# Optimization experiments

Hardware: AMD Instinct MI355X
Metric: run time of the kernel (lower is better)

Reference implementation:

```python
import jax, jax.numpy as jnp
import numpy as np
import math

LMAX = 2            # input lmax
LMAX_OUT = 2 * LMAX # gaunt product output lmax
RES_BETA = 20
RES_ALPHA = 39
N = 2048
MUL = 64
C = 64
BRANCHES = [(1, 1), (1, -1), (-1, 1)]  # (p_val1, p_val2) per branch


def _real_sh_grid(lmax, res_beta, res_alpha):
    """Real orthonormal spherical harmonics on a Gauss-Legendre x uniform-alpha grid.
    Returns Y [(lmax+1)^2, res_beta, res_alpha] and quadrature weights qw [res_beta]
    (beta GL weight times 2*pi/res_alpha alpha weight)."""
    x, w = np.polynomial.legendre.leggauss(res_beta)  # x = cos(beta)
    phi = np.linspace(0.0, 2.0 * np.pi, res_alpha, endpoint=False)
    # associated Legendre P[l, m] on x via standard recurrences
    P = np.zeros((lmax + 1, lmax + 1, res_beta))
    P[0, 0] = 1.0
    s = np.sqrt(1.0 - x ** 2)
    for m in range(1, lmax + 1):
        P[m, m] = -(2 * m - 1) * s * P[m - 1, m - 1]
    for m in range(lmax):
        P[m + 1, m] = (2 * m + 1) * x * P[m, m]
    for m in range(lmax + 1):
        for l in range(m + 2, lmax + 1):
            P[l, m] = ((2 * l - 1) * x * P[l - 1, m] - (l + m - 1) * P[l - 2, m]) / (l - m)
    Y = np.zeros(((lmax + 1) ** 2, res_beta, res_alpha))
    idx = 0
    for l in range(lmax + 1):
        for m in range(-l, l + 1):
            am = abs(m)
            K = math.sqrt((2 * l + 1) / (4 * math.pi) * math.factorial(l - am) / math.factorial(l + am))
            if m == 0:
                ang = np.ones(res_alpha)
            elif m > 0:
                ang = math.sqrt(2.0) * np.cos(m * phi)
            else:
                ang = math.sqrt(2.0) * np.sin(am * phi)
            Y[idx] = K * P[l, am][:, None] * ang[None, :]
            idx += 1
    qw = w * (2.0 * np.pi / res_alpha)
    return Y.astype(np.float32), qw.astype(np.float32)


def setup_inputs() -> dict:
    key = jax.random.key(0)
    k1, k2, k3, k4, k5 = jax.random.split(key, 5)
    # inputs carry both parities per l: [N, mul, parity(2), (lmax+1)^2]
    x1 = jax.random.normal(k1, (N, MUL, 2, (LMAX + 1) ** 2), dtype=jnp.float32)
    x2 = jax.random.normal(k2, (N, MUL, 2, (LMAX + 1) ** 2), dtype=jnp.float32)
    # per-branch, per-l linear weights (e3nn Linear mixes multiplicities within each irrep)
    W1 = jax.random.normal(k3, (3, LMAX + 1, MUL, C), dtype=jnp.float32)
    W2 = jax.random.normal(k4, (3, LMAX + 1, MUL, C), dtype=jnp.float32)
    Wout = jax.random.normal(k5, (3, LMAX_OUT + 1, C, C), dtype=jnp.float32)
    Yfull, qw = _real_sh_grid(LMAX_OUT, RES_BETA, RES_ALPHA)
    Y_in = jnp.asarray(Yfull[: (LMAX + 1) ** 2])   # [9, B, A]
    Y_out = jnp.asarray(Yfull)                     # [25, B, A]
    return {"x1": x1, "x2": x2, "W1": W1, "W2": W2, "Wout": Wout,
            "Y_in": Y_in, "Y_out": Y_out, "qw": jnp.asarray(qw)}


def _project(x, W, p_val):
    """e3nn Linear to s2_irreps(LMAX, p_val)*C: for each l, take the input block with
    parity p_val*(-1)^l and mix multiplicities. x [N,mul,2,L2], W [L, mul, C] -> [N, C, L2]."""
    blocks = []
    inv_sqrt_mul = 1.0 / np.sqrt(x.shape[1])
    for l in range(LMAX + 1):
        pidx = 0 if p_val * ((-1) ** l) == 1 else 1  # 0 = even, 1 = odd parity slot
        sl = slice(l * l, (l + 1) * (l + 1))
        blocks.append(jnp.einsum('nmk,mc->nck', x[:, :, pidx, sl], W[l]) * inv_sqrt_mul)
    return jnp.concatenate(blocks, axis=-1)  # [N, C, (LMAX+1)^2]


def _gaunt_branch(x1, x2, W1b, W2b, Woutb, p1, p2, Y_in, Y_out, qw):
    c1 = _project(x1, W1b, p1)                      # [N, C, 9]
    c2 = _project(x2, W2b, p2)
    # SH -> grid (inverse spherical transform)
    s1 = jnp.einsum('ncl,lba->ncba', c1, Y_in)      # [N, C, B, A]
    s2 = jnp.einsum('ncl,lba->ncba', c2, Y_in)
    # pointwise multiply on S2, then grid -> SH (forward transform w/ quadrature)
    co = jnp.einsum('ncba,lba,b->ncl', s1 * s2, Y_out, qw)  # [N, C, 25]
    # linear_out: per-l [C -> C] mixing
    inv_sqrt_c = 1.0 / np.sqrt(co.shape[1])
    outs = []
    for l in range(LMAX_OUT + 1):
        sl = slice(l * l, (l + 1) * (l + 1))
        outs.append(jnp.einsum('nck,cd->ndk', co[:, :, sl], Woutb[l]) * inv_sqrt_c)
    return jnp.concatenate(outs, axis=-1)           # [N, C, 25]


def reference(x1, x2, W1, W2, Wout, Y_in, Y_out, qw):
    outs = [_gaunt_branch(x1, x2, W1[b], W2[b], Wout[b], p1, p2, Y_in, Y_out, qw)
            for b, (p1, p2) in enumerate(BRANCHES)]
    return jnp.stack(outs, axis=1)                  # [N, 3, C, 25] (concat over parities)
```

## Files before the change

kernel.cpp:

```cpp
#include <hip/hip_runtime.h>
#include <utility>


#define NN 2048

__host__ __device__ constexpr int l_of9(int i)  { return i < 1 ? 0 : (i < 4 ? 1 : 2); }
__host__ __device__ constexpr int l_of25(int k) { return k < 1 ? 0 : (k < 4 ? 1 : (k < 9 ? 2 : (k < 16 ? 3 : 4))); }
__host__ __device__ constexpr int iabs_(int v)  { return v < 0 ? -v : v; }

__host__ __device__ constexpr bool gmask(int k, int i, int j) {
    const int l3 = l_of25(k), m3 = k - l3 * l3 - l3;
    const int l1 = l_of9(i),  m1 = i - l1 * l1 - l1;
    const int l2 = l_of9(j),  m2 = j - l2 * l2 - l2;
    if (((l1 + l2 + l3) & 1) != 0) return false;
    if (l3 > l1 + l2 || l3 < iabs_(l1 - l2)) return false;
    const int am3 = iabs_(m3);
    return (am3 == iabs_(m1 + m2)) || (am3 == iabs_(m1 - m2));
}

struct GTab {
    int po[82];
    int pc[81];
    int kl[81][12];
    constexpr GTab() : po{}, pc{}, kl{} {
        int off = 0;
        for (int ij = 0; ij < 81; ++ij) {
            po[ij] = off;
            const int i = ij / 9, j = ij % 9;
            int cnum = 0;
            for (int k = 0; k < 25; ++k)
                if (gmask(k, i, j)) kl[ij][cnum++] = k;
            pc[ij] = cnum;
            off += (cnum + 3) & ~3;
        }
        po[81] = off;
    }
};
constexpr GTab GT{};

__global__ __launch_bounds__(256) void gaunt_pack_kernel(
    const float* __restrict__ Y_in, const float* __restrict__ Y_out,
    const float* __restrict__ qw, float* __restrict__ gp)
{
    const int ij = blockIdx.x;
    const int i = ij / 9, j = ij % 9;
    const int t = threadIdx.x;

    __shared__ float yy[780];
    __shared__ float ps[25][8];
    __shared__ float gr[25];

    for (int p = t; p < 780; p += 256)
        yy[p] = Y_in[i * 780 + p] * Y_in[j * 780 + p] * qw[p / 39];
    __syncthreads();

    if (t < 200) {
        const int k = t >> 3, s = t & 7;
        const float* yo = Y_out + k * 780;
        const int p1 = (s * 98 + 98 < 780) ? (s * 98 + 98) : 780;
        float a = 0.f;
        for (int p = s * 98; p < p1; ++p) a = fmaf(yy[p], yo[p], a);
        ps[k][s] = a;
    }
    __syncthreads();

    if (t < 25) {
        float a = 0.f;
#pragma unroll
        for (int s = 0; s < 8; ++s) a += ps[t][s];
        gr[t] = a;
    }
    __syncthreads();

    const int cntp = (GT.pc[ij] + 3) & ~3;
    if (t < cntp)
        gp[GT.po[ij] + t] = (t < GT.pc[ij]) ? gr[GT.kl[ij][t]] : 0.f;
}

template <int IJ, int... Ts>
__device__ __forceinline__ void gaunt_apply(const float (&g)[12], float pij,
    float (&cov)[25], std::integer_sequence<int, Ts...>)
{
    ((cov[GT.kl[IJ][Ts]] = fmaf(g[Ts], pij, cov[GT.kl[IJ][Ts]])), ...);
}

template <int IJ>
__device__ __forceinline__ void gaunt_pair(const float* __restrict__ gp,
    const float (&c1)[9], const float (&c2)[9], float (&cov)[25])
{
    constexpr int cnt = GT.pc[IJ];
    if constexpr (cnt > 0) {
        constexpr int base = GT.po[IJ];
        constexpr int nv = (cnt + 3) / 4;
        const float pij = c1[IJ / 9] * c2[IJ % 9];
        float g[12];
#pragma unroll
        for (int q = 0; q < nv; ++q) {
            const float4 v = ((const float4*)(gp + base))[q];
            g[4 * q] = v.x; g[4 * q + 1] = v.y; g[4 * q + 2] = v.z; g[4 * q + 3] = v.w;
        }
        gaunt_apply<IJ>(g, pij, cov, std::make_integer_sequence<int, cnt>{});
    }
}

template <int I, int... Js>
__device__ __forceinline__ void gaunt_row(const float* __restrict__ gp,
    const float (&c1)[9], const float (&c2)[9], float (&cov)[25],
    std::integer_sequence<int, Js...>)
{
    (gaunt_pair<I * 9 + Js>(gp, c1, c2, cov), ...);
    __builtin_amdgcn_sched_barrier(0);
}

template <int... Is>
__device__ __forceinline__ void gaunt_all(const float* __restrict__ gp,
    const float (&c1)[9], const float (&c2)[9], float (&cov)[25],
    std::integer_sequence<int, Is...>)
{
    (gaunt_row<Is>(gp, c1, c2, cov, std::make_integer_sequence<int, 9>{}), ...);
}

template <int E1, int E2>
__device__ __forceinline__ void fused_body(
    const float* __restrict__ x1, const float* __restrict__ x2,
    const float* __restrict__ W1, const float* __restrict__ W2,
    const float* __restrict__ Wout, const float* __restrict__ gp,
    float* __restrict__ out, char* smem, int b)
{
    const int t = threadIdx.x;
    const int c = t & 63;
    const int w = t >> 6;
    const int n = blockIdx.x * 4 + w;

    float2* ws = (float2*)smem;
    float*  cs2 = (float*)smem;
    float*  cs  = (float*)(smem + 25600);

    const float* x1n = x1 + (size_t)n * 1152;
    const float* x2n = x2 + (size_t)n * 1152;

    float a1[9] = {0,0,0,0,0,0,0,0,0};
    float a2[9] = {0,0,0,0,0,0,0,0,0};

    for (int mc = 0; mc < 4; ++mc) {
        if (mc) __syncthreads();
        for (int idx = t; idx < 3072; idx += 256) {
            const int l = idx >> 10;
            const int r = idx & 1023;
            const int gi = ((b * 3 + l) * 64 + (mc * 16 + (r >> 6))) * 64 + (r & 63);
            ws[idx] = make_float2(W1[gi], W2[gi]);
        }
        __syncthreads();

#pragma unroll 1
        for (int mp = 0; mp < 8; ++mp) {
            const int m0 = mc * 16 + mp * 2;
            const float4* p1 = (const float4*)(x1n + m0 * 18);
            const float4* p2 = (const float4*)(x2n + m0 * 18);
            float xs1[36], xs2[36];
#pragma unroll
            for (int q = 0; q < 9; ++q) {
                const float4 t1 = p1[q], t2 = p2[q];
                xs1[4*q] = t1.x; xs1[4*q+1] = t1.y; xs1[4*q+2] = t1.z; xs1[4*q+3] = t1.w;
                xs2[4*q] = t2.x; xs2[4*q+1] = t2.y; xs2[4*q+2] = t2.z; xs2[4*q+3] = t2.w;
            }
            float2 wv[3][2];
#pragma unroll
            for (int l = 0; l < 3; ++l)
#pragma unroll
                for (int mi = 0; mi < 2; ++mi)
                    wv[l][mi] = ws[(l * 16 + mp * 2 + mi) * 64 + c];
#pragma unroll
            for (int l = 0; l < 3; ++l) {
                const int O1 = ((l & 1) ^ E1) * 9 + l * l;
                const int O2 = ((l & 1) ^ E2) * 9 + l * l;
#pragma unroll
                for (int mi = 0; mi < 2; ++mi)
#pragma unroll
                    for (int ii = 0; ii <= 2 * l; ++ii) {
                        a1[l*l+ii] = fmaf(xs1[O1 + 18*mi + ii], wv[l][mi].x, a1[l*l+ii]);
                        a2[l*l+ii] = fmaf(xs2[O2 + 18*mi + ii], wv[l][mi].y, a2[l*l+ii]);
                    }
            }
        }
    }
    __syncthreads();

    float c1[9], c2[9];
#pragma unroll
    for (int i = 0; i < 9; ++i) { c1[i] = a1[i] * 0.125f; c2[i] = a2[i] * 0.125f; }

    float cov[25] = {0,0,0,0,0,0,0,0,0,0,0,0,0,0,0,0,0,0,0,0,0,0,0,0,0};
    gaunt_all(gp, c1, c2, cov, std::make_integer_sequence<int, 9>{});

    float* csw = cs + w * (64 * 20);
    const float* WoB = Wout + (size_t)b * 5 * 4096 + c;

#pragma unroll
    for (int kk = 0; kk < 13; ++kk) csw[c * 20 + kk] = cov[kk];
    float accA[13];
#pragma unroll
    for (int kk = 0; kk < 13; ++kk) accA[kk] = 0.f;
#pragma unroll 2
    for (int d = 0; d < 64; ++d) {
        const float4 cv0 = *(const float4*)&csw[d * 20 + 0];
        const float4 cv1 = *(const float4*)&csw[d * 20 + 4];
        const float4 cv2 = *(const float4*)&csw[d * 20 + 8];
        const float4 cv3 = *(const float4*)&csw[d * 20 + 12];
        const float wv0 = WoB[(0 * 64 + d) * 64];
        const float wv1 = WoB[(1 * 64 + d) * 64];
        const float wv2 = WoB[(2 * 64 + d) * 64];
        const float wv3 = WoB[(3 * 64 + d) * 64];
        accA[0]  = fmaf(cv0.x, wv0, accA[0]);
        accA[1]  = fmaf(cv0.y, wv1, accA[1]);
        accA[2]  = fmaf(cv0.z, wv1, accA[2]);
        accA[3]  = fmaf(cv0.w, wv1, accA[3]);
        accA[4]  = fmaf(cv1.x, wv2, accA[4]);
        accA[5]  = fmaf(cv1.y, wv2, accA[5]);
        accA[6]  = fmaf(cv1.z, wv2, accA[6]);
        accA[7]  = fmaf(cv1.w, wv2, accA[7]);
        accA[8]  = fmaf(cv2.x, wv2, accA[8]);
        accA[9]  = fmaf(cv2.y, wv3, accA[9]);
        accA[10] = fmaf(cv2.z, wv3, accA[10]);
        accA[11] = fmaf(cv2.w, wv3, accA[11]);
        accA[12] = fmaf(cv3.x, wv3, accA[12]);
    }
#pragma unroll
    for (int kk = 0; kk < 13; ++kk)
        cs2[w * 1600 + c * 25 + kk] = accA[kk] * 0.125f;

#pragma unroll
    for (int kk = 0; kk < 12; ++kk) csw[c * 20 + kk] = cov[13 + kk];
    float accB[12];
#pragma unroll
    for (int kk = 0; kk < 12; ++kk) accB[kk] = 0.f;
#pragma unroll 2
    for (int d = 0; d < 64; ++d) {
        const float4 cv0 = *(const float4*)&csw[d * 20 + 0];
        const float4 cv1 = *(const float4*)&csw[d * 20 + 4];
        const float4 cv2 = *(const float4*)&csw[d * 20 + 8];
        const float wv3 = WoB[(3 * 64 + d) * 64];
        const float wv4 = WoB[(4 * 64 + d) * 64];
        accB[0]  = fmaf(cv0.x, wv3, accB[0]);
        accB[1]  = fmaf(cv0.y, wv3, accB[1]);
        accB[2]  = fmaf(cv0.z, wv3, accB[2]);
        accB[3]  = fmaf(cv0.w, wv4, accB[3]);
        accB[4]  = fmaf(cv1.x, wv4, accB[4]);
        accB[5]  = fmaf(cv1.y, wv4, accB[5]);
        accB[6]  = fmaf(cv1.z, wv4, accB[6]);
        accB[7]  = fmaf(cv1.w, wv4, accB[7]);
        accB[8]  = fmaf(cv2.x, wv4, accB[8]);
        accB[9]  = fmaf(cv2.y, wv4, accB[9]);
        accB[10] = fmaf(cv2.z, wv4, accB[10]);
        accB[11] = fmaf(cv2.w, wv4, accB[11]);
    }
#pragma unroll
    for (int kk = 0; kk < 12; ++kk)
        cs2[w * 1600 + c * 25 + 13 + kk] = accB[kk] * 0.125f;

    float* outn = out + ((size_t)n * 3 + b) * 1600;
#pragma unroll
    for (int r = 0; r < 6; ++r) {
        const float4 v = *(const float4*)&cs2[w * 1600 + r * 256 + c * 4];
        *(float4*)&outn[r * 256 + c * 4] = v;
    }
    outn[1536 + c] = cs2[w * 1600 + 1536 + c];
}

__global__ __launch_bounds__(256) void fused_kernel(
    const float* __restrict__ x1, const float* __restrict__ x2,
    const float* __restrict__ W1, const float* __restrict__ W2,
    const float* __restrict__ Wout, const float* __restrict__ gp,
    float* __restrict__ out)
{
    __shared__ __align__(16) char smem[46080];
    const int b = blockIdx.y;
    if (b == 0)      fused_body<0, 0>(x1, x2, W1, W2, Wout, gp, out, smem, 0);
    else if (b == 1) fused_body<0, 1>(x1, x2, W1, W2, Wout, gp, out, smem, 1);
    else             fused_body<1, 0>(x1, x2, W1, W2, Wout, gp, out, smem, 2);
}

extern "C" void kernel_launch(void* const* d_in, const int* in_sizes, int n_in,
                              void* d_out, int out_size, void* d_ws, size_t ws_size,
                              hipStream_t stream) {
    const float* x1    = (const float*)d_in[0];
    const float* x2    = (const float*)d_in[1];
    const float* W1    = (const float*)d_in[2];
    const float* W2    = (const float*)d_in[3];
    const float* Wout  = (const float*)d_in[4];
    const float* Y_in  = (const float*)d_in[5];
    const float* Y_out = (const float*)d_in[6];
    const float* qw    = (const float*)d_in[7];
    float* outp = (float*)d_out;
    float* gp   = (float*)d_ws;

    gaunt_pack_kernel<<<81, 256, 0, stream>>>(Y_in, Y_out, qw, gp);
    fused_kernel<<<dim3(NN / 4, 3), 256, 0, stream>>>(x1, x2, W1, W2, Wout, gp, outp);
}
```

Baseline: 157.8 us.

## Drop shared-memory weight staging, read W1/W2 directly, single-pass output projection

Removes the cooperative LDS staging of W1/W2 and its block-wide barriers, so each thread reads its weight column straight from global memory (cached in L2). The output linear stage becomes one 25-wide accumulation pass over a padded per-wave shared buffer instead of two passes, and results are written directly to global without an LDS transpose. Shared memory shrinks from 45 KB to 28 KB and launch bounds request 5 blocks per CU to raise occupancy. The trade-off is more register pressure from 25 accumulators and uncoalesced per-thread 25-float output stores.

```diff
diff --git a/kernel.cpp b/kernel.cpp
--- a/kernel.cpp
+++ b/kernel.cpp
@@ -125,66 +125,54 @@
     const float* __restrict__ x1, const float* __restrict__ x2,
     const float* __restrict__ W1, const float* __restrict__ W2,
     const float* __restrict__ Wout, const float* __restrict__ gp,
-    float* __restrict__ out, char* smem, int b)
+    float* __restrict__ out, float* __restrict__ cs, int b)
 {
     const int t = threadIdx.x;
     const int c = t & 63;
-    const int w = t >> 6;
+    const int w = __builtin_amdgcn_readfirstlane(t >> 6);
     const int n = blockIdx.x * 4 + w;
-
-    float2* ws = (float2*)smem;
-    float*  cs2 = (float*)smem;
-    float*  cs  = (float*)(smem + 25600);
 
     const float* x1n = x1 + (size_t)n * 1152;
     const float* x2n = x2 + (size_t)n * 1152;
+    const float* W1b = W1 + (size_t)b * 3 * 4096 + c;
+    const float* W2b = W2 + (size_t)b * 3 * 4096 + c;
 
     float a1[9] = {0,0,0,0,0,0,0,0,0};
     float a2[9] = {0,0,0,0,0,0,0,0,0};
 
-    for (int mc = 0; mc < 4; ++mc) {
-        if (mc) __syncthreads();
-        for (int idx = t; idx < 3072; idx += 256) {
-            const int l = idx >> 10;
-            const int r = idx & 1023;
-            const int gi = ((b * 3 + l) * 64 + (mc * 16 + (r >> 6))) * 64 + (r & 63);
-            ws[idx] = make_float2(W1[gi], W2[gi]);
-        }
-        __syncthreads();
-
 #pragma unroll 1
-        for (int mp = 0; mp < 8; ++mp) {
-            const int m0 = mc * 16 + mp * 2;
-            const float4* p1 = (const float4*)(x1n + m0 * 18);
-            const float4* p2 = (const float4*)(x2n + m0 * 18);
-            float xs1[36], xs2[36];
-#pragma unroll
-            for (int q = 0; q < 9; ++q) {
-                const float4 t1 = p1[q], t2 = p2[q];
-                xs1[4*q] = t1.x; xs1[4*q+1] = t1.y; xs1[4*q+2] = t1.z; xs1[4*q+3] = t1.w;
-                xs2[4*q] = t2.x; xs2[4*q+1] = t2.y; xs2[4*q+2] = t2.z; xs2[4*q+3] = t2.w;
+    for (int mp = 0; mp < 32; ++mp) {
+        const float4* p1 = (const float4*)(x1n + mp * 36);
+        const float4* p2 = (const float4*)(x2n + mp * 36);
+        float xs1[36], xs2[36];
+#pragma unroll
+        for (int q = 0; q < 9; ++q) {
+            const float4 t1 = p1[q], t2 = p2[q];
+            xs1[4*q] = t1.x; xs1[4*q+1] = t1.y; xs1[4*q+2] = t1.z; xs1[4*q+3] = t1.w;
+            xs2[4*q] = t2.x; xs2[4*q+1] = t2.y; xs2[4*q+2] = t2.z; xs2[4*q+3] = t2.w;
+        }
+        float w1v[3][2], w2v[3][2];
+#pragma unroll
+        for (int l = 0; l < 3; ++l)
+#pragma unroll
+            for (int mi = 0; mi < 2; ++mi) {
+                const int moff = (l * 64 + mp * 2 + mi) * 64;
+                w1v[l][mi] = W1b[moff];
+                w2v[l][mi] = W2b[moff];
             }
-            float2 wv[3][2];
-#pragma unroll
-            for (int l = 0; l < 3; ++l)
-#pragma unroll
-                for (int mi = 0; mi < 2; ++mi)
-                    wv[l][mi] = ws[(l * 16 + mp * 2 + mi) * 64 + c];
-#pragma unroll
-            for (int l = 0; l < 3; ++l) {
-                const int O1 = ((l & 1) ^ E1) * 9 + l * l;
-                const int O2 = ((l & 1) ^ E2) * 9 + l * l;
-#pragma unroll
-                for (int mi = 0; mi < 2; ++mi)
-#pragma unroll
-                    for (int ii = 0; ii <= 2 * l; ++ii) {
-                        a1[l*l+ii] = fmaf(xs1[O1 + 18*mi + ii], wv[l][mi].x, a1[l*l+ii]);
-                        a2[l*l+ii] = fmaf(xs2[O2 + 18*mi + ii], wv[l][mi].y, a2[l*l+ii]);
-                    }
-            }
-        }
-    }
-    __syncthreads();
+#pragma unroll
+        for (int l = 0; l < 3; ++l) {
+            const int O1 = ((l & 1) ^ E1) * 9 + l * l;
+            const int O2 = ((l & 1) ^ E2) * 9 + l * l;
+#pragma unroll
+            for (int mi = 0; mi < 2; ++mi)
+#pragma unroll
+                for (int ii = 0; ii <= 2 * l; ++ii) {
+                    a1[l*l+ii] = fmaf(xs1[O1 + 18*mi + ii], w1v[l][mi], a1[l*l+ii]);
+                    a2[l*l+ii] = fmaf(xs2[O2 + 18*mi + ii], w2v[l][mi], a2[l*l+ii]);
+                }
+        }
+    }
 
     float c1[9], c2[9];
 #pragma unroll
@@ -193,91 +181,47 @@
     float cov[25] = {0,0,0,0,0,0,0,0,0,0,0,0,0,0,0,0,0,0,0,0,0,0,0,0,0};
     gaunt_all(gp, c1, c2, cov, std::make_integer_sequence<int, 9>{});
 
-    float* csw = cs + w * (64 * 20);
+    float* csw = cs + w * (64 * 28);
+#pragma unroll
+    for (int kk = 0; kk < 25; ++kk) csw[c * 28 + kk] = cov[kk];
+
     const float* WoB = Wout + (size_t)b * 5 * 4096 + c;
-
-#pragma unroll
-    for (int kk = 0; kk < 13; ++kk) csw[c * 20 + kk] = cov[kk];
-    float accA[13];
-#pragma unroll
-    for (int kk = 0; kk < 13; ++kk) accA[kk] = 0.f;
-#pragma unroll 2
+    float acc[25];
+#pragma unroll
+    for (int kk = 0; kk < 25; ++kk) acc[kk] = 0.f;
+
+#pragma unroll 1
     for (int d = 0; d < 64; ++d) {
-        const float4 cv0 = *(const float4*)&csw[d * 20 + 0];
-        const float4 cv1 = *(const float4*)&csw[d * 20 + 4];
-        const float4 cv2 = *(const float4*)&csw[d * 20 + 8];
-        const float4 cv3 = *(const float4*)&csw[d * 20 + 12];
-        const float wv0 = WoB[(0 * 64 + d) * 64];
-        const float wv1 = WoB[(1 * 64 + d) * 64];
-        const float wv2 = WoB[(2 * 64 + d) * 64];
-        const float wv3 = WoB[(3 * 64 + d) * 64];
-        accA[0]  = fmaf(cv0.x, wv0, accA[0]);
-        accA[1]  = fmaf(cv0.y, wv1, accA[1]);
-        accA[2]  = fmaf(cv0.z, wv1, accA[2]);
-        accA[3]  = fmaf(cv0.w, wv1, accA[3]);
-        accA[4]  = fmaf(cv1.x, wv2, accA[4]);
-        accA[5]  = fmaf(cv1.y, wv2, accA[5]);
-        accA[6]  = fmaf(cv1.z, wv2, accA[6]);
-        accA[7]  = fmaf(cv1.w, wv2, accA[7]);
-        accA[8]  = fmaf(cv2.x, wv2, accA[8]);
-        accA[9]  = fmaf(cv2.y, wv3, accA[9]);
-        accA[10] = fmaf(cv2.z, wv3, accA[10]);
-        accA[11] = fmaf(cv2.w, wv3, accA[11]);
-        accA[12] = fmaf(cv3.x, wv3, accA[12]);
-    }
-#pragma unroll
-    for (int kk = 0; kk < 13; ++kk)
-        cs2[w * 1600 + c * 25 + kk] = accA[kk] * 0.125f;
-
-#pragma unroll
-    for (int kk = 0; kk < 12; ++kk) csw[c * 20 + kk] = cov[13 + kk];
-    float accB[12];
-#pragma unroll
-    for (int kk = 0; kk < 12; ++kk) accB[kk] = 0.f;
-#pragma unroll 2
-    for (int d = 0; d < 64; ++d) {
-        const float4 cv0 = *(const float4*)&csw[d * 20 + 0];
-        const float4 cv1 = *(const float4*)&csw[d * 20 + 4];
-        const float4 cv2 = *(const float4*)&csw[d * 20 + 8];
-        const float wv3 = WoB[(3 * 64 + d) * 64];
-        const float wv4 = WoB[(4 * 64 + d) * 64];
-        accB[0]  = fmaf(cv0.x, wv3, accB[0]);
-        accB[1]  = fmaf(cv0.y, wv3, accB[1]);
-        accB[2]  = fmaf(cv0.z, wv3, accB[2]);
-        accB[3]  = fmaf(cv0.w, wv4, accB[3]);
-        accB[4]  = fmaf(cv1.x, wv4, accB[4]);
-        accB[5]  = fmaf(cv1.y, wv4, accB[5]);
-        accB[6]  = fmaf(cv1.z, wv4, accB[6]);
-        accB[7]  = fmaf(cv1.w, wv4, accB[7]);
-        accB[8]  = fmaf(cv2.x, wv4, accB[8]);
-        accB[9]  = fmaf(cv2.y, wv4, accB[9]);
-        accB[10] = fmaf(cv2.z, wv4, accB[10]);
-        accB[11] = fmaf(cv2.w, wv4, accB[11]);
-    }
-#pragma unroll
-    for (int kk = 0; kk < 12; ++kk)
-        cs2[w * 1600 + c * 25 + 13 + kk] = accB[kk] * 0.125f;
-
-    float* outn = out + ((size_t)n * 3 + b) * 1600;
-#pragma unroll
-    for (int r = 0; r < 6; ++r) {
-        const float4 v = *(const float4*)&cs2[w * 1600 + r * 256 + c * 4];
-        *(float4*)&outn[r * 256 + c * 4] = v;
-    }
-    outn[1536 + c] = cs2[w * 1600 + 1536 + c];
-}
-
-__global__ __launch_bounds__(256) void fused_kernel(
+        float row[28];
+#pragma unroll
+        for (int q = 0; q < 7; ++q) {
+            const float4 v = *(const float4*)&csw[d * 28 + 4 * q];
+            row[4*q] = v.x; row[4*q+1] = v.y; row[4*q+2] = v.z; row[4*q+3] = v.w;
+        }
+        float wv[5];
+#pragma unroll
+        for (int l3 = 0; l3 < 5; ++l3) wv[l3] = WoB[(l3 * 64 + d) * 64];
+#pragma unroll
+        for (int k = 0; k < 25; ++k)
+            acc[k] = fmaf(row[k], wv[l_of25(k)], acc[k]);
+    }
+
+    float* op = out + (((size_t)n * 3 + b) * 64 + c) * 25;
+#pragma unroll
+    for (int k = 0; k < 25; ++k) op[k] = acc[k] * 0.125f;
+}
+
+__global__ __launch_bounds__(256, 5) void fused_kernel(
     const float* __restrict__ x1, const float* __restrict__ x2,
     const float* __restrict__ W1, const float* __restrict__ W2,
     const float* __restrict__ Wout, const float* __restrict__ gp,
     float* __restrict__ out)
 {
-    __shared__ __align__(16) char smem[46080];
+    __shared__ __align__(16) float cs[4 * 64 * 28];
     const int b = blockIdx.y;
-    if (b == 0)      fused_body<0, 0>(x1, x2, W1, W2, Wout, gp, out, smem, 0);
-    else if (b == 1) fused_body<0, 1>(x1, x2, W1, W2, Wout, gp, out, smem, 1);
-    else             fused_body<1, 0>(x1, x2, W1, W2, Wout, gp, out, smem, 2);
+    if (b == 0)      fused_body<0, 0>(x1, x2, W1, W2, Wout, gp, out, cs, 0);
+    else if (b == 1) fused_body<0, 1>(x1, x2, W1, W2, Wout, gp, out, cs, 1);
+    else             fused_body<1, 0>(x1, x2, W1, W2, Wout, gp, out, cs, 2);
 }
 
 extern "C" void kernel_launch(void* const* d_in, const int* in_sizes, int n_in,
```

Result: faster. 141.6 us (-10.3%).
